# Optimization experiments

Hardware: AMD Instinct MI355X
Metric: run time of the kernel (lower is better)

The kernel has to match this reference:

```python
import jax, jax.numpy as jnp
import numpy as np

S, B, D = 1024, 2, 1024      # seq, batch, embed_dim
E, TOPK = 15, 3              # routed experts = 8*2-1, top_n = 2*2-1
F = 1024                     # per-expert ffn dim (ffn_dim // m)
FS = 2048                    # shared expert ffn dim (ffn_dim * n_shared)


def _uinit(k, shape, out_dim):
    std = out_dim ** -0.5
    return jax.random.uniform(k, shape, jnp.float32, -std, std)


def setup_inputs() -> dict:
    key = jax.random.key(0)
    ks = jax.random.split(key, 10)
    return {
        "x": jax.random.normal(ks[0], (S, B, D), jnp.float32),
        "gate_w": jax.random.normal(ks[1], (E, D), jnp.float32) * (D ** -0.5),
        "fc1_w": _uinit(ks[2], (E, 2 * F, D), 2 * F),
        "fc1_b": _uinit(ks[3], (E, 2 * F), 2 * F),
        "geglu_mult": jnp.ones((E, F), jnp.float32),
        "fc2_w": _uinit(ks[4], (E, D, F), D),
        "fc2_b": _uinit(ks[5], (E, D), D),
        "s_fc1_w": _uinit(ks[6], (2 * FS, D), 2 * FS),
        "s_fc1_b": _uinit(ks[7], (2 * FS,), 2 * FS),
        "s_geglu_mult": jnp.ones((FS,), jnp.float32),
        "s_fc2_w": _uinit(ks[8], (D, FS), D),
        "s_fc2_b": _uinit(ks[9], (D,), D),
    }


def reference(x, gate_w, fc1_w, fc1_b, geglu_mult, fc2_w, fc2_b,
              s_fc1_w, s_fc1_b, s_geglu_mult, s_fc2_w, s_fc2_b):
    s, b, d = x.shape
    xt = x.reshape(-1, d)                              # [T, D] tokens
    T = xt.shape[0]

    # --- gate: softmax over routed experts, top-k, renormalize ---
    logits = xt @ gate_w.T                             # [T, E]
    scores = jax.nn.softmax(logits, axis=-1)
    topk_w, topk_idx = jax.lax.top_k(scores, TOPK)     # [T, K]
    topk_w = topk_w / (jnp.sum(topk_w, axis=-1, keepdims=True) + 1e-20)
    # combine weights: zero for non-routed experts (same math as dispatch/scatter)
    comb = jnp.zeros((T, E), xt.dtype).at[jnp.arange(T)[:, None], topk_idx].add(topk_w)

    # --- routed experts: GEGLU FFN applied as grouped GEMM, weighted combine ---
    h = jnp.einsum('td,efd->etf', xt, fc1_w) + fc1_b[:, None, :]   # [E, T, 2F]
    xh, g = h[..., :F], h[..., F:]                                 # chunk: (x, gate)
    a = jax.nn.gelu(g, approximate=False) * xh * geglu_mult[:, None, :]
    yexp = jnp.einsum('etf,edf->etd', a, fc2_w) + fc2_b[:, None, :]  # [E, T, D]
    y = jnp.einsum('etd,te->td', yexp, comb)                         # [T, D]

    # --- shared expert ---
    hs = xt @ s_fc1_w.T + s_fc1_b                      # [T, 2*FS]
    xs, gs = hs[..., :FS], hs[..., FS:]
    as_ = jax.nn.gelu(gs, approximate=False) * xs * s_geglu_mult
    ys = as_ @ s_fc2_w.T + s_fc2_b                     # [T, D]

    return (y + ys).reshape(s, b, d)
```

## Files before the change

kernel.cpp:

```cpp
#include <hip/hip_runtime.h>

typedef __attribute__((ext_vector_type(8))) short bfrag;
typedef __attribute__((ext_vector_type(4))) float f32x4;

__device__ __forceinline__ short f2bf(float f) {
  union { float f; unsigned u; } v; v.f = f;
  unsigned r = v.u + 0x7FFFu + ((v.u >> 16) & 1u);
  return (short)(r >> 16);
}
__device__ __forceinline__ float bf2f(unsigned short h) {
  union { unsigned u; float f; } v; v.u = ((unsigned)h) << 16;
  return v.f;
}
__device__ __forceinline__ float gelu_exact(float g) {
  return 0.5f * g * (1.0f + erff(g * 0.70710678118654752f));
}
__device__ __forceinline__ void gld_lds16(const short* g, short* l) {
  __builtin_amdgcn_global_load_lds(
      (const __attribute__((address_space(1))) void*)g,
      (__attribute__((address_space(3))) void*)l, 16, 0, 0);
}

__global__ __launch_bounds__(256) void k_convert_w(
    const float* __restrict__ s0, const float* __restrict__ s1,
    const float* __restrict__ s2, const float* __restrict__ s3,
    short* __restrict__ d0, short* __restrict__ d1,
    short* __restrict__ d2, short* __restrict__ d3)
{
  const int b = blockIdx.x;
  const float* s; short* d; long off;
  if (b < 3840)      { s = s0; d = d0; off = (long)b * 2048; }
  else if (b < 5760) { s = s1; d = d1; off = (long)(b - 3840) * 2048; }
  else if (b < 6272) { s = s2; d = d2; off = (long)(b - 5760) * 2048; }
  else               { s = s3; d = d3; off = (long)(b - 6272) * 2048; }
  const f32x4* sp = (const f32x4*)s;
  const long i0 = off + threadIdx.x;
  f32x4 v[8];
#pragma unroll
  for (int j = 0; j < 8; j++) v[j] = __builtin_nontemporal_load(sp + i0 + j * 256);
#pragma unroll
  for (int j = 0; j < 8; j++)
    ((short4*)d)[i0 + j * 256] =
        make_short4(f2bf(v[j].x), f2bf(v[j].y), f2bf(v[j].z), f2bf(v[j].w));
}

__global__ __launch_bounds__(64) void k_gate(const float* __restrict__ x,
    const float* __restrict__ gw, int* __restrict__ topk_idx,
    float* __restrict__ topk_w, short* __restrict__ xbf)
{
  const int t0 = blockIdx.x * 4;
  const int lane = threadIdx.x;
  float xv[4][16];
#pragma unroll
  for (int tt = 0; tt < 4; tt++)
#pragma unroll
    for (int i = 0; i < 16; i++) {
      xv[tt][i] = x[(size_t)(t0 + tt) * 1024 + lane + 64 * i];
      xbf[(size_t)(t0 + tt) * 1024 + lane + 64 * i] = f2bf(xv[tt][i]);
    }
  float p[4][15];
#pragma unroll
  for (int e = 0; e < 15; e++) {
    float wv[16];
#pragma unroll
    for (int i = 0; i < 16; i++) wv[i] = gw[(size_t)e * 1024 + lane + 64 * i];
#pragma unroll
    for (int tt = 0; tt < 4; tt++) {
      float s = 0.f;
#pragma unroll
      for (int i = 0; i < 16; i++) s += xv[tt][i] * wv[i];
#pragma unroll
      for (int o = 32; o; o >>= 1) s += __shfl_xor(s, o, 64);
      p[tt][e] = s;
    }
  }
#pragma unroll
  for (int tt = 0; tt < 4; tt++) {
    float m = -1e30f;
#pragma unroll
    for (int e = 0; e < 15; e++) m = fmaxf(m, p[tt][e]);
    float q[15], Z = 0.f;
#pragma unroll
    for (int e = 0; e < 15; e++) { q[e] = expf(p[tt][e] - m); Z += q[e]; }
    int usedMask = 0; int bi[3]; float bv[3];
#pragma unroll
    for (int j = 0; j < 3; j++) {
      float best = -1.f; int b = 0;
#pragma unroll
      for (int e = 0; e < 15; e++) {
        bool ok = (!((usedMask >> e) & 1)) && (q[e] > best);
        if (ok) { best = q[e]; b = e; }
      }
      bi[j] = b; bv[j] = best / Z; usedMask |= 1 << b;
    }
    if (lane == tt) {
      float den = bv[0] + bv[1] + bv[2] + 1e-20f;
#pragma unroll
      for (int j = 0; j < 3; j++) {
        topk_idx[(t0 + tt) * 3 + j] = bi[j];
        topk_w[(t0 + tt) * 3 + j] = bv[j] / den;
      }
    }
  }
}

__global__ __launch_bounds__(1024) void k_route(const int* __restrict__ topk_idx,
    const float* __restrict__ topk_w, int* __restrict__ cnt_g, int* __restrict__ offs_g,
    int* __restrict__ row_tok, float* __restrict__ row_wt, int* __restrict__ row_id)
{
  __shared__ int scnt[16], soffs[16], sfill[16];
  const int tid = threadIdx.x;
  if (tid < 16) { scnt[tid] = 0; sfill[tid] = 0; }
  __syncthreads();
  for (int i = tid; i < 6144; i += 1024) atomicAdd(&scnt[topk_idx[i]], 1);
  __syncthreads();
  if (tid == 0) {
    int a = 0;
    for (int e = 0; e < 15; e++) { soffs[e] = a; offs_g[e] = a; cnt_g[e] = scnt[e]; a += scnt[e]; }
  }
  __syncthreads();
  for (int i = tid; i < 6144; i += 1024) {
    int e = topk_idx[i];
    int pos = atomicAdd(&sfill[e], 1);
    int row = soffs[e] + pos;
    row_tok[row] = i / 3;
    row_wt[row] = topk_w[i];
    row_id[i] = row;
  }
}

__device__ __forceinline__ bool resolve_tile256(const int* __restrict__ cnt, int ty,
                                                int& e, int& lt) {
  int acc = 0;
#pragma unroll
  for (int i = 0; i < 15; i++) {
    int tl = (cnt[i] + 255) >> 8;
    if (ty < acc + tl) { e = i; lt = ty - acc; return true; }
    acc += tl;
  }
  return false;
}

__global__ __launch_bounds__(512, 2) void k_fc1(
    const short* __restrict__ xbf,
    const short* __restrict__ wsh, const float* __restrict__ bsh, const float* __restrict__ msh,
    const short* __restrict__ wex, const float* __restrict__ bex, const float* __restrict__ mex,
    const int* __restrict__ cnt, const int* __restrict__ offs, const int* __restrict__ row_tok,
    short* __restrict__ as_buf, short* __restrict__ a_buf)
{
  __shared__ short smem[2 * 32768];
  const int tid = threadIdx.x;
  const int bid = blockIdx.x;
  const bool sh = bid < 128;
  int f0, m0 = 0, e = 0, rowBase = 0, nrows = 256;
  if (sh) {
    f0 = (bid & 15) * 128; m0 = (bid >> 4) * 256;
  } else {
    const int b2 = bid - 128;
    int lt;
    if (!resolve_tile256(cnt, b2 >> 3, e, lt)) return;
    f0 = (b2 & 7) * 128;
    rowBase = offs[e] + lt * 256;
    nrows = cnt[e] - lt * 256; if (nrows > 256) nrows = 256;
  }
  const int lane = tid & 63, ml = lane & 15, kq = lane >> 4, mlo = lane & 7;
  const int wv = tid >> 6, wr = wv >> 2, wc = wv & 3;
  const int lrow = lane >> 3, lchk = lane & 7;
  const int Fhalf = sh ? 2048 : 1024;
  const short* wptr = sh ? wsh : (wex + (size_t)e * 2048 * 1024);
  const short* aSrc[4]; const short* bSrc[4];
#pragma unroll
  for (int t = 0; t < 4; t++) {
    const int r = wv * 32 + t * 8 + lrow;
    const int sc = (lchk ^ (r & 7)) * 8;
    if (sh) aSrc[t] = xbf + (size_t)(m0 + r) * 1024 + sc;
    else {
      const int rc = r < nrows ? r : nrows - 1;
      aSrc[t] = xbf + (size_t)row_tok[rowBase + rc] * 1024 + sc;
    }
    const int grow = (r < 128) ? (f0 + r) : (Fhalf + f0 + r - 128);
    bSrc[t] = wptr + (size_t)grow * 1024 + sc;
  }
  f32x4 acc[8][4] = {};

#define FC1_STAGE(BUF, K0) do {                                              \
    short* A_ = smem + (BUF) * 32768;                                        \
    short* B_ = A_ + 16384;                                                  \
    _Pragma("unroll")                                                        \
    for (int t = 0; t < 4; t++) gld_lds16(aSrc[t] + (K0), A_ + (wv * 32 + t * 8) * 64); \
    _Pragma("unroll")                                                        \
    for (int t = 0; t < 4; t++) gld_lds16(bSrc[t] + (K0), B_ + (wv * 32 + t * 8) * 64); \
  } while (0)

#define FC1_COMPUTE(BUF) do {                                                \
    const short* As_ = smem + (BUF) * 32768;                                 \
    const short* Bs_ = As_ + 16384;                                          \
    _Pragma("unroll")                                                        \
    for (int kk = 0; kk < 2; kk++) {                                         \
      const int so = ((kk * 4 + kq) ^ mlo) * 8;                              \
      bfrag af[8], bb[4];                                                    \
      _Pragma("unroll")                                                      \
      for (int i = 0; i < 8; i++)                                            \
        af[i] = *(const bfrag*)&As_[(wr * 128 + i * 16 + ml) * 64 + so];     \
      _Pragma("unroll")                                                      \
      for (int j = 0; j < 4; j++) {                                          \
        const int brow = (j >> 1) * 128 + wc * 32 + (j & 1) * 16 + ml;       \
        bb[j] = *(const bfrag*)&Bs_[brow * 64 + so];                         \
      }                                                                      \
      _Pragma("unroll")                                                      \
      for (int i = 0; i < 8; i++)                                            \
        _Pragma("unroll")                                                    \
        for (int j = 0; j < 4; j++)                                          \
          acc[i][j] = __builtin_amdgcn_mfma_f32_16x16x32_bf16(af[i], bb[j], acc[i][j], 0, 0, 0); \
    }                                                                        \
  } while (0)

  FC1_STAGE(0, 0);
  for (int ks = 0; ks < 16; ks++) {
    if (ks < 15) {
      FC1_STAGE((ks + 1) & 1, (ks + 1) * 64);
      asm volatile("s_waitcnt vmcnt(8)" ::: "memory");
    } else {
      asm volatile("s_waitcnt vmcnt(0)" ::: "memory");
    }
    __builtin_amdgcn_sched_barrier(0);
    __builtin_amdgcn_s_barrier();
    __builtin_amdgcn_sched_barrier(0);
    FC1_COMPUTE(ks & 1);
    __builtin_amdgcn_s_barrier();
    __builtin_amdgcn_sched_barrier(0);
  }

  const float* bias = sh ? bsh : (bex + (size_t)e * 2048);
  const float* mult = sh ? msh : (mex + (size_t)e * 1024);
#pragma unroll
  for (int jj = 0; jj < 2; jj++) {
    const int fl = wc * 32 + jj * 16 + ml;
    const int f = f0 + fl;
    const float b1 = bias[f];
    const float b2 = bias[Fhalf + f];
    const float mv = mult[f];
#pragma unroll
    for (int i = 0; i < 8; i++)
#pragma unroll
      for (int rg = 0; rg < 4; rg++) {
        const int row = wr * 128 + i * 16 + kq * 4 + rg;
        const float h1 = acc[i][jj][rg] + b1;
        const float h2 = acc[i][jj + 2][rg] + b2;
        const short o = f2bf(gelu_exact(h2) * h1 * mv);
        if (sh) as_buf[(size_t)(m0 + row) * 2048 + f] = o;
        else if (row < nrows) a_buf[(size_t)(rowBase + row) * 1024 + f] = o;
      }
  }
}

__global__ __launch_bounds__(512, 2) void k_fc2(
    const short* __restrict__ as_buf, const short* __restrict__ wsfc2, const float* __restrict__ s_b,
    const short* __restrict__ a_buf, const short* __restrict__ wfc2, const float* __restrict__ e_b,
    const int* __restrict__ cnt, const int* __restrict__ offs, const float* __restrict__ row_wt,
    float* __restrict__ y, short* __restrict__ yexp)
{
  __shared__ short smem[2 * 24576];
  const int tid = threadIdx.x;
  const int bid = blockIdx.x;
  const bool sh = bid < 64;
  int d0, m0 = 0, e = 0, rowBase = 0, nrows = 256, Klen, astr, bstr;
  const short *aBase, *bBase;
  if (sh) {
    d0 = (bid & 7) * 128; m0 = (bid >> 3) * 256;
    Klen = 2048; astr = 2048; bstr = 2048;
    aBase = as_buf; bBase = wsfc2;
  } else {
    const int b2 = bid - 64;
    int lt;
    if (!resolve_tile256(cnt, b2 >> 3, e, lt)) return;
    d0 = (b2 & 7) * 128;
    rowBase = offs[e] + lt * 256;
    nrows = cnt[e] - lt * 256; if (nrows > 256) nrows = 256;
    Klen = 1024; astr = 1024; bstr = 1024;
    aBase = a_buf + (size_t)rowBase * 1024;
    bBase = wfc2 + (size_t)e * 1024 * 1024;
  }
  const int lane = tid & 63, ml = lane & 15, kq = lane >> 4, mlo = lane & 7;
  const int wv = tid >> 6, wr = wv >> 2, wc = wv & 3;
  const int lrow = lane >> 3, lchk = lane & 7;
  const short* aSrc[4]; const short* bSrc[2];
#pragma unroll
  for (int t = 0; t < 4; t++) {
    const int r = wv * 32 + t * 8 + lrow;
    const int sc = (lchk ^ (r & 7)) * 8;
    const int rc = (sh || r < nrows) ? r : nrows - 1;
    aSrc[t] = aBase + (size_t)(sh ? (m0 + r) : rc) * astr + sc;
  }
#pragma unroll
  for (int t = 0; t < 2; t++) {
    const int rb = wv * 16 + t * 8 + lrow;
    const int sc = (lchk ^ (rb & 7)) * 8;
    bSrc[t] = bBase + (size_t)(d0 + rb) * bstr + sc;
  }
  f32x4 acc[8][2] = {};

#define FC2_STAGE(BUF, K0) do {                                              \
    short* A_ = smem + (BUF) * 24576;                                        \
    short* B_ = A_ + 16384;                                                  \
    _Pragma("unroll")                                                        \
    for (int t = 0; t < 4; t++) gld_lds16(aSrc[t] + (K0), A_ + (wv * 32 + t * 8) * 64); \
    _Pragma("unroll")                                                        \
    for (int t = 0; t < 2; t++) gld_lds16(bSrc[t] + (K0), B_ + (wv * 16 + t * 8) * 64); \
  } while (0)

#define FC2_COMPUTE(BUF) do {                                                \
    const short* As_ = smem + (BUF) * 24576;                                 \
    const short* Bs_ = As_ + 16384;                                          \
    _Pragma("unroll")                                                        \
    for (int kk = 0; kk < 2; kk++) {                                         \
      const int so = ((kk * 4 + kq) ^ mlo) * 8;                              \
      bfrag af[8], bb[2];                                                    \
      _Pragma("unroll")                                                      \
      for (int i = 0; i < 8; i++)                                            \
        af[i] = *(const bfrag*)&As_[(wr * 128 + i * 16 + ml) * 64 + so];     \
      _Pragma("unroll")                                                      \
      for (int j = 0; j < 2; j++)                                            \
        bb[j] = *(const bfrag*)&Bs_[(wc * 32 + j * 16 + ml) * 64 + so];      \
      _Pragma("unroll")                                                      \
      for (int i = 0; i < 8; i++)                                            \
        _Pragma("unroll")                                                    \
        for (int j = 0; j < 2; j++)                                          \
          acc[i][j] = __builtin_amdgcn_mfma_f32_16x16x32_bf16(af[i], bb[j], acc[i][j], 0, 0, 0); \
    }                                                                        \
  } while (0)

  FC2_STAGE(0, 0);
  const int NK = Klen >> 6;
  for (int ks = 0; ks < NK; ks++) {
    if (ks < NK - 1) {
      FC2_STAGE((ks + 1) & 1, (ks + 1) * 64);
      asm volatile("s_waitcnt vmcnt(6)" ::: "memory");
    } else {
      asm volatile("s_waitcnt vmcnt(0)" ::: "memory");
    }
    __builtin_amdgcn_sched_barrier(0);
    __builtin_amdgcn_s_barrier();
    __builtin_amdgcn_sched_barrier(0);
    FC2_COMPUTE(ks & 1);
    __builtin_amdgcn_s_barrier();
    __builtin_amdgcn_sched_barrier(0);
  }

#pragma unroll
  for (int j = 0; j < 2; j++) {
    const int d = d0 + wc * 32 + j * 16 + ml;
    const float bv = sh ? s_b[d] : e_b[(size_t)e * 1024 + d];
#pragma unroll
    for (int i = 0; i < 8; i++)
#pragma unroll
      for (int rg = 0; rg < 4; rg++) {
        const int row = wr * 128 + i * 16 + kq * 4 + rg;
        if (sh) {
          y[(size_t)(m0 + row) * 1024 + d] = acc[i][j][rg] + bv;
        } else if (row < nrows) {
          const float wt = row_wt[rowBase + row];
          yexp[(size_t)(rowBase + row) * 1024 + d] = f2bf((acc[i][j][rg] + bv) * wt);
        }
      }
  }
}

__global__ __launch_bounds__(256) void k_combine(float* __restrict__ y,
    const short* __restrict__ yexp, const int* __restrict__ row_id)
{
  const int idx = blockIdx.x * 256 + threadIdx.x;
  const int t = idx >> 8;
  const int d4 = (idx & 255) * 4;
  const int r0 = row_id[t * 3], r1 = row_id[t * 3 + 1], r2 = row_id[t * 3 + 2];
  float4 acc = *(float4*)(y + (size_t)t * 1024 + d4);
  const ushort4 v0 = *(const ushort4*)(yexp + (size_t)r0 * 1024 + d4);
  const ushort4 v1 = *(const ushort4*)(yexp + (size_t)r1 * 1024 + d4);
  const ushort4 v2 = *(const ushort4*)(yexp + (size_t)r2 * 1024 + d4);
  acc.x += bf2f(v0.x) + bf2f(v1.x) + bf2f(v2.x);
  acc.y += bf2f(v0.y) + bf2f(v1.y) + bf2f(v2.y);
  acc.z += bf2f(v0.z) + bf2f(v1.z) + bf2f(v2.z);
  acc.w += bf2f(v0.w) + bf2f(v1.w) + bf2f(v2.w);
  *(float4*)(y + (size_t)t * 1024 + d4) = acc;
}

extern "C" void kernel_launch(void* const* d_in, const int* in_sizes, int n_in,
                              void* d_out, int out_size, void* d_ws, size_t ws_size,
                              hipStream_t stream) {
  const float* x          = (const float*)d_in[0];
  const float* gate_w     = (const float*)d_in[1];
  const float* fc1_w      = (const float*)d_in[2];
  const float* fc1_b      = (const float*)d_in[3];
  const float* geglu_mult = (const float*)d_in[4];
  const float* fc2_w      = (const float*)d_in[5];
  const float* fc2_b      = (const float*)d_in[6];
  const float* s_fc1_w    = (const float*)d_in[7];
  const float* s_fc1_b    = (const float*)d_in[8];
  const float* s_mult     = (const float*)d_in[9];
  const float* s_fc2_w    = (const float*)d_in[10];
  const float* s_fc2_b    = (const float*)d_in[11];
  float* y = (float*)d_out;

  char* wsb = (char*)d_ws;
  int*   cnt      = (int*)(wsb + 0);
  int*   offs     = (int*)(wsb + 64);
  int*   topk_idx = (int*)(wsb + 256);
  float* topk_w   = (float*)(wsb + 24832);
  int*   row_tok  = (int*)(wsb + 49408);
  float* row_wt   = (float*)(wsb + 74496);
  int*   row_id   = (int*)(wsb + 99584);
  short* xbf      = (short*)(wsb + 131072);
  short* a_buf    = (short*)(wsb + 8519680);
  short* as_buf   = (short*)(wsb + 21364736);
  short* yexp     = (short*)(wsb + 29753344);
  short* wbf_sfc1 = (short*)(wsb + 42598400);
  short* wbf_sfc2 = (short*)(wsb + 50987008);
  short* wbf_fc1  = (short*)(wsb + 55181312);
  short* wbf_fc2  = (short*)(wsb + 118095872);

  k_convert_w<<<6528, 256, 0, stream>>>(fc1_w, fc2_w, s_fc1_w, s_fc2_w,
                                        wbf_fc1, wbf_fc2, wbf_sfc1, wbf_sfc2);
  k_gate<<<512, 64, 0, stream>>>(x, gate_w, topk_idx, topk_w, xbf);
  k_route<<<1, 1024, 0, stream>>>(topk_idx, topk_w, cnt, offs, row_tok, row_wt, row_id);
  k_fc1<<<440, 512, 0, stream>>>(xbf, wbf_sfc1, s_fc1_b, s_mult,
                                 wbf_fc1, fc1_b, geglu_mult,
                                 cnt, offs, row_tok, as_buf, a_buf);
  k_fc2<<<376, 512, 0, stream>>>(as_buf, wbf_sfc2, s_fc2_b,
                                 a_buf, wbf_fc2, fc2_b,
                                 cnt, offs, row_wt, y, yexp);
  k_combine<<<2048, 256, 0, stream>>>(y, yexp, row_id);
}
```

Before: 422.9 us.

## Stage weight tiles through registers to overlap loads with MFMA compute

B (weight) tiles in both GEMM kernels are now loaded into registers before compute and written to LDS after compute, instead of being fetched with direct global-to-LDS loads. The A tile still uses global_load_lds. Each iteration now has one barrier, with the vmcnt wait moved after the MFMA block, so global latency is meant to hide behind compute instead of stalling before the barrier. The cost is extra VGPRs, explicit LDS writes, and a full vmcnt(0) wait for the A loads as well.

New measurement: 560.0 us. +32.4%, slower.

```diff
diff --git a/kernel.cpp b/kernel.cpp
--- a/kernel.cpp
+++ b/kernel.cpp
@@ -182,14 +182,24 @@
     bSrc[t] = wptr + (size_t)grow * 1024 + sc;
   }
   f32x4 acc[8][4] = {};
-
-#define FC1_STAGE(BUF, K0) do {                                              \
+  int4 br[4];
+
+#define FC1_ASTAGE(BUF, K0) do {                                             \
     short* A_ = smem + (BUF) * 32768;                                        \
-    short* B_ = A_ + 16384;                                                  \
     _Pragma("unroll")                                                        \
     for (int t = 0; t < 4; t++) gld_lds16(aSrc[t] + (K0), A_ + (wv * 32 + t * 8) * 64); \
-    _Pragma("unroll")                                                        \
-    for (int t = 0; t < 4; t++) gld_lds16(bSrc[t] + (K0), B_ + (wv * 32 + t * 8) * 64); \
+  } while (0)
+
+#define FC1_BLOAD(K0) do {                                                   \
+    _Pragma("unroll")                                                        \
+    for (int t = 0; t < 4; t++) br[t] = *(const int4*)(bSrc[t] + (K0));      \
+  } while (0)
+
+#define FC1_BWRITE(BUF) do {                                                 \
+    short* B_ = smem + (BUF) * 32768 + 16384;                                \
+    _Pragma("unroll")                                                        \
+    for (int t = 0; t < 4; t++)                                              \
+      *(int4*)&B_[(wv * 32 + t * 8 + lrow) * 64 + lchk * 8] = br[t];         \
   } while (0)
 
 #define FC1_COMPUTE(BUF) do {                                                \
@@ -215,18 +225,27 @@
     }                                                                        \
   } while (0)
 
-  FC1_STAGE(0, 0);
+  FC1_ASTAGE(0, 0);
+  FC1_BLOAD(0);
+  asm volatile("s_waitcnt vmcnt(0)" ::: "memory");
+  FC1_BWRITE(0);
+  asm volatile("s_waitcnt lgkmcnt(0)" ::: "memory");
+  __builtin_amdgcn_s_barrier();
+  __builtin_amdgcn_sched_barrier(0);
+
   for (int ks = 0; ks < 16; ks++) {
     if (ks < 15) {
-      FC1_STAGE((ks + 1) & 1, (ks + 1) * 64);
-      asm volatile("s_waitcnt vmcnt(8)" ::: "memory");
-    } else {
-      asm volatile("s_waitcnt vmcnt(0)" ::: "memory");
-    }
-    __builtin_amdgcn_sched_barrier(0);
-    __builtin_amdgcn_s_barrier();
+      FC1_ASTAGE((ks + 1) & 1, (ks + 1) * 64);
+      FC1_BLOAD((ks + 1) * 64);
+    }
     __builtin_amdgcn_sched_barrier(0);
     FC1_COMPUTE(ks & 1);
+    if (ks < 15) {
+      asm volatile("s_waitcnt vmcnt(0)" ::: "memory");
+      __builtin_amdgcn_sched_barrier(0);
+      FC1_BWRITE((ks + 1) & 1);
+    }
+    asm volatile("s_waitcnt lgkmcnt(0)" ::: "memory");
     __builtin_amdgcn_s_barrier();
     __builtin_amdgcn_sched_barrier(0);
   }
@@ -299,14 +318,24 @@
     bSrc[t] = bBase + (size_t)(d0 + rb) * bstr + sc;
   }
   f32x4 acc[8][2] = {};
-
-#define FC2_STAGE(BUF, K0) do {                                              \
+  int4 br[2];
+
+#define FC2_ASTAGE(BUF, K0) do {                                             \
     short* A_ = smem + (BUF) * 24576;                                        \
-    short* B_ = A_ + 16384;                                                  \
     _Pragma("unroll")                                                        \
     for (int t = 0; t < 4; t++) gld_lds16(aSrc[t] + (K0), A_ + (wv * 32 + t * 8) * 64); \
-    _Pragma("unroll")                                                        \
-    for (int t = 0; t < 2; t++) gld_lds16(bSrc[t] + (K0), B_ + (wv * 16 + t * 8) * 64); \
+  } while (0)
+
+#define FC2_BLOAD(K0) do {                                                   \
+    _Pragma("unroll")                                                        \
+    for (int t = 0; t < 2; t++) br[t] = *(const int4*)(bSrc[t] + (K0));      \
+  } while (0)
+
+#define FC2_BWRITE(BUF) do {                                                 \
+    short* B_ = smem + (BUF) * 24576 + 16384;                                \
+    _Pragma("unroll")                                                        \
+    for (int t = 0; t < 2; t++)                                              \
+      *(int4*)&B_[(wv * 16 + t * 8 + lrow) * 64 + lchk * 8] = br[t];         \
   } while (0)
 
 #define FC2_COMPUTE(BUF) do {                                                \
@@ -330,19 +359,28 @@
     }                                                                        \
   } while (0)
 
-  FC2_STAGE(0, 0);
+  FC2_ASTAGE(0, 0);
+  FC2_BLOAD(0);
+  asm volatile("s_waitcnt vmcnt(0)" ::: "memory");
+  FC2_BWRITE(0);
+  asm volatile("s_waitcnt lgkmcnt(0)" ::: "memory");
+  __builtin_amdgcn_s_barrier();
+  __builtin_amdgcn_sched_barrier(0);
+
   const int NK = Klen >> 6;
   for (int ks = 0; ks < NK; ks++) {
     if (ks < NK - 1) {
-      FC2_STAGE((ks + 1) & 1, (ks + 1) * 64);
-      asm volatile("s_waitcnt vmcnt(6)" ::: "memory");
-    } else {
-      asm volatile("s_waitcnt vmcnt(0)" ::: "memory");
-    }
-    __builtin_amdgcn_sched_barrier(0);
-    __builtin_amdgcn_s_barrier();
+      FC2_ASTAGE((ks + 1) & 1, (ks + 1) * 64);
+      FC2_BLOAD((ks + 1) * 64);
+    }
     __builtin_amdgcn_sched_barrier(0);
     FC2_COMPUTE(ks & 1);
+    if (ks < NK - 1) {
+      asm volatile("s_waitcnt vmcnt(0)" ::: "memory");
+      __builtin_amdgcn_sched_barrier(0);
+      FC2_BWRITE((ks + 1) & 1);
+    }
+    asm volatile("s_waitcnt lgkmcnt(0)" ::: "memory");
     __builtin_amdgcn_s_barrier();
     __builtin_amdgcn_sched_barrier(0);
   }
```
